# Kernel tuning notes

Measured on AMD Instinct MI355X. Metric: run time of the kernel, lower is better.

The kernel has to match this reference:

```python
import jax, jax.numpy as jnp
import numpy as np

N_NODES = 100000
N_EDGES = 3200000
HIDDEN = 128
N_CLASSES = 10
N_GRAPHS = 128
EPS = 1e-5


def setup_inputs() -> dict:
    key = jax.random.key(0)
    ks = jax.random.split(key, 16)
    x = jax.random.normal(ks[0], (N_NODES, 1), dtype=jnp.float32)
    edge_index = jax.random.randint(ks[1], (2, N_EDGES), 0, N_NODES, dtype=jnp.int64)
    batch = jnp.sort(jax.random.randint(ks[2], (N_NODES,), 0, N_GRAPHS, dtype=jnp.int64))
    def lin(k, fi, fo):
        s = 1.0 / np.sqrt(fi)
        return jax.random.uniform(k, (fi, fo), jnp.float32, -s, s)
    return {
        "x": x, "edge_index": edge_index, "batch": batch,
        "Wc1": lin(ks[3], 1, HIDDEN), "bc1": jnp.zeros((HIDDEN,), jnp.float32),
        "Wl1": lin(ks[4], 1, HIDDEN), "bl1": jnp.zeros((HIDDEN,), jnp.float32),
        "g1": jnp.ones((HIDDEN,), jnp.float32), "be1": jnp.zeros((HIDDEN,), jnp.float32),
        "Wc2": lin(ks[5], HIDDEN, HIDDEN), "bc2": jnp.zeros((HIDDEN,), jnp.float32),
        "Wl2": lin(ks[6], HIDDEN, HIDDEN), "bl2": jnp.zeros((HIDDEN,), jnp.float32),
        "g2": jnp.ones((HIDDEN,), jnp.float32), "be2": jnp.zeros((HIDDEN,), jnp.float32),
        "W3": lin(ks[7], HIDDEN, N_CLASSES), "b3": jnp.zeros((N_CLASSES,), jnp.float32),
    }


def _gcn_conv(x, W, b, src, dst, n):
    # PyG GCNConv: add self-loops, symmetric normalization, then scatter-add.
    h = x @ W                                    # [N, F]
    loops = jnp.arange(n, dtype=src.dtype)
    s = jnp.concatenate([src, loops])
    d = jnp.concatenate([dst, loops])
    deg = jax.ops.segment_sum(jnp.ones_like(d, dtype=h.dtype), d, num_segments=n)
    dinv = jnp.where(deg > 0, jax.lax.rsqrt(deg), 0.0)
    norm = dinv[s] * dinv[d]                     # [E+N]
    msg = h[s] * norm[:, None]                   # gather + scale
    out = jax.ops.segment_sum(msg, d, num_segments=n)
    return out + b


def _batch_norm(x, gamma, beta):
    mu = jnp.mean(x, axis=0)
    var = jnp.mean(jnp.square(x - mu), axis=0)
    return (x - mu) * jax.lax.rsqrt(var + EPS) * gamma + beta


def reference(x, edge_index, batch, Wc1, bc1, Wl1, bl1, g1, be1,
              Wc2, bc2, Wl2, bl2, g2, be2, W3, b3):
    src, dst = edge_index[0], edge_index[1]
    n = x.shape[0]
    h = _gcn_conv(x, Wc1, bc1, src, dst, n) + (x @ Wl1 + bl1)
    h = jax.nn.relu(h)
    h = _batch_norm(h, g1, be1)
    h = _gcn_conv(h, Wc2, bc2, src, dst, n) + (h @ Wl2 + bl2)
    h = _batch_norm(h, g2, be2)
    # global_mean_pool over graph ids
    sums = jax.ops.segment_sum(h, batch, num_segments=N_GRAPHS)
    cnts = jax.ops.segment_sum(jnp.ones((n,), h.dtype), batch, num_segments=N_GRAPHS)
    pooled = sums / jnp.maximum(cnts, 1.0)[:, None]
    return pooled @ W3 + b3
```

## Files before the change

kernel.cpp:

```cpp
#include <hip/hip_runtime.h>
#include <hip/hip_bf16.h>

__device__ __forceinline__ float bf2f(unsigned short u) {
    union { unsigned int i; float f; } c; c.i = ((unsigned int)u) << 16; return c.f;
}
__device__ __forceinline__ unsigned short f2bf(float f) {
    union { unsigned int i; float f; } c; c.f = f;
    unsigned int i = c.i;
    unsigned int r = (i + 0x7FFFu + ((i >> 16) & 1u)) >> 16;
    return (unsigned short)r;
}
__device__ __forceinline__ float u2f_hi(unsigned int u) {
    union { unsigned int i; float f; } c; c.i = u & 0xFFFF0000u; return c.f;
}
__device__ __forceinline__ float u2f_lo(unsigned int u) {
    union { unsigned int i; float f; } c; c.i = u << 16; return c.f;
}
__device__ __forceinline__ int ldi(const void* p, long long i, int is64) {
    return is64 ? (int)((const long long*)p)[i] : ((const int*)p)[i];
}

typedef __attribute__((ext_vector_type(8))) short short8;
typedef __attribute__((ext_vector_type(4))) float floatx4;

#define HID 128
#define EPS 1e-5f
#define NBK 256
#define CH 4096

#define OF_WC1 0
#define OF_BC1 128
#define OF_WL1 256
#define OF_BL1 384
#define OF_G1  512
#define OF_BE1 640
#define OF_WC2 768
#define OF_BC2 17152
#define OF_WL2 17280
#define OF_BL2 33664
#define OF_G2  33792
#define OF_BE2 33920
#define OF_W3  34048
#define OF_B3  35328
#define N_CANON 35338

__global__ void k_zero(int* __restrict__ p, long long n,
                       const unsigned int* __restrict__ g1w,
                       const unsigned int* __restrict__ eiw,
                       int* __restrict__ flags) {
    long long i = (long long)blockIdx.x * blockDim.x + threadIdx.x;
    if (i < n) p[i] = 0;
    if (blockIdx.x == 0 && threadIdx.x == 0) {
        flags[0] = (g1w[0] == 0x3F800000u) ? 1 : 0;
        flags[1] = (eiw[1] == 0u && eiw[3] == 0u && eiw[5] == 0u) ? 1 : 0;
    }
}

struct ConvArgs { const void* s[14]; float* d[14]; int n[14]; };
__global__ void k_wconv(ConvArgs a, const int* __restrict__ flags,
                        unsigned short* __restrict__ W2T) {
    int seg = blockIdx.y;
    int i = blockIdx.x * 256 + threadIdx.x;
    if (i >= a.n[seg]) return;
    float v = flags[0] ? ((const float*)a.s[seg])[i]
                       : bf2f(((const unsigned short*)a.s[seg])[i]);
    a.d[seg][i] = v;
    if (seg == 6) W2T[(i & 127) * 256 + (i >> 7)] = f2bf(v);
    else if (seg == 8) W2T[(i & 127) * 256 + 128 + (i >> 7)] = f2bf(v);
}


__global__ void __launch_bounds__(256) k_bhist(const void* __restrict__ ei, int E, int N,
                                               const int* __restrict__ flags,
                                               int* __restrict__ bcnt) {
    __shared__ int h[NBK];
    int t = threadIdx.x;
    h[t] = 0;
    __syncthreads();
    int is64 = flags[1];
    long long base = (long long)blockIdx.x * CH;
    for (int k = 0; k < CH / 256; k++) {
        long long i = base + k * 256 + t;
        if (i < E) {
            int d = ldi(ei, (long long)E + i, is64);
            if ((unsigned)d < (unsigned)N) atomicAdd(&h[d >> 9], 1);
        }
    }
    __syncthreads();
    if (h[t]) atomicAdd(&bcnt[t], h[t]);
}

__global__ void k_bscan(const int* __restrict__ bcnt, int* __restrict__ boff,
                        int* __restrict__ bcur) {
    __shared__ int sd[NBK];
    int t = threadIdx.x;
    int v = bcnt[t];
    sd[t] = v;
    __syncthreads();
    for (int off = 1; off < NBK; off <<= 1) {
        int add = (t >= off) ? sd[t - off] : 0;
        __syncthreads();
        sd[t] += add;
        __syncthreads();
    }
    int ex = sd[t] - v;
    boff[t] = ex;
    bcur[t] = ex;
}

__global__ void __launch_bounds__(256) k_bpart(const void* __restrict__ ei, int E, int N,
                                               const int* __restrict__ flags,
                                               int* __restrict__ bcur, uint2* __restrict__ pairs) {
    __shared__ uint2 buf[CH];
    __shared__ int h[NBK], sc[NBK], offs[NBK], cur[NBK], gpos[NBK];
    int t = threadIdx.x;
    h[t] = 0;
    __syncthreads();
    int is64 = flags[1];
    long long base = (long long)blockIdx.x * CH;
    int ss[CH / 256], dd[CH / 256];
    bool ok[CH / 256];
#pragma unroll
    for (int k = 0; k < CH / 256; k++) {
        long long i = base + k * 256 + t;
        ok[k] = false; ss[k] = 0; dd[k] = 0;
        if (i < E) {
            int s = ldi(ei, i, is64);
            int d = ldi(ei, (long long)E + i, is64);
            ss[k] = s; dd[k] = d;
            if ((unsigned)s < (unsigned)N && (unsigned)d < (unsigned)N) {
                ok[k] = true;
                atomicAdd(&h[d >> 9], 1);
            }
        }
    }
    __syncthreads();
    int hv = h[t];
    sc[t] = hv;
    __syncthreads();
    for (int off = 1; off < NBK; off <<= 1) {
        int add = (t >= off) ? sc[t - off] : 0;
        __syncthreads();
        sc[t] += add;
        __syncthreads();
    }
    offs[t] = sc[t] - hv;
    cur[t] = sc[t] - hv;
    __syncthreads();
#pragma unroll
    for (int k = 0; k < CH / 256; k++) {
        if (ok[k]) {
            int b = dd[k] >> 9;
            int p = atomicAdd(&cur[b], 1);
            buf[p] = make_uint2((unsigned)ss[k], (unsigned)dd[k]);
        }
    }
    if (hv) gpos[t] = atomicAdd(&bcur[t], hv);
    else gpos[t] = 0;
    __syncthreads();
    int vc = offs[NBK - 1] + h[NBK - 1];
    for (int i = t; i < vc; i += 256) {
        uint2 e = buf[i];
        int lo = (int)(e.y >> 9);
        pairs[(size_t)gpos[lo] + (i - offs[lo])] = e;
    }
}

__global__ void __launch_bounds__(256) k_bcsr(const uint2* __restrict__ pairs,
                                              const int* __restrict__ boff,
                                              const int* __restrict__ bcnt,
                                              const void* __restrict__ x,
                                              const int* __restrict__ flags,
                                              int N, int E,
                                              int* __restrict__ deg, int* __restrict__ rowptr,
                                              int* __restrict__ col,
                                              float* __restrict__ dinv, float* __restrict__ xf,
                                              float* __restrict__ xd1) {
    __shared__ int cnt[512], lofs[512], lcur[512], part[256];
    int b = blockIdx.x, t = threadIdx.x;
    for (int j = t; j < 512; j += 256) { cnt[j] = 0; lcur[j] = 0; }
    __syncthreads();
    int s0 = boff[b], n = bcnt[b];
    for (int i = t; i < n; i += 256) {
        uint2 p = pairs[(size_t)s0 + i];
        atomicAdd(&cnt[p.y & 511], 1);
    }
    __syncthreads();
    int a0 = cnt[2 * t], a1 = cnt[2 * t + 1];
    part[t] = a0 + a1;
    __syncthreads();
    for (int off = 1; off < 256; off <<= 1) {
        int add = (t >= off) ? part[t - off] : 0;
        __syncthreads();
        part[t] += add;
        __syncthreads();
    }
    int ex = part[t] - (a0 + a1);
    lofs[2 * t] = ex;
    lofs[2 * t + 1] = ex + a0;
    __syncthreads();
    int vb = b << 9;
    int isf32 = flags[0];
    for (int j = t; j < 512; j += 256) {
        int v = vb + j;
        if (v < N) {
            int dg = cnt[j];
            deg[v] = dg;
            rowptr[v] = s0 + lofs[j];
            float dv = rsqrtf((float)(dg + 1));
            float xv = isf32 ? ((const float*)x)[v] : bf2f(((const unsigned short*)x)[v]);
            dinv[v] = dv;
            xf[v] = xv;
            xd1[v] = xv * dv;
        }
    }
    for (int i = t; i < n; i += 256) {
        uint2 p = pairs[(size_t)s0 + i];
        int dl = p.y & 511;
        int sl = atomicAdd(&lcur[dl], 1);
        int idx = s0 + lofs[dl] + sl;
        if ((unsigned)idx < (unsigned)E) col[idx] = (int)p.x;
    }
}

__global__ void __launch_bounds__(256) k_bps(const uint2* __restrict__ pairs,
                                             const int* __restrict__ boff,
                                             const int* __restrict__ bcnt,
                                             const float* __restrict__ xd1,
                                             const float* __restrict__ xf,
                                             const float* __restrict__ dinv,
                                             const float* __restrict__ C,
                                             int N, float4* __restrict__ node,
                                             float* __restrict__ S1a, float* __restrict__ S2a) {
    __shared__ float psL[512], xL[512];
    int b = blockIdx.x, t = threadIdx.x;
    for (int j = t; j < 512; j += 256) psL[j] = 0.f;
    __syncthreads();
    int s0 = boff[b], n = bcnt[b];
    for (int i = t; i < n; i += 256) {
        uint2 p = pairs[(size_t)s0 + i];
        atomicAdd(&psL[p.y & 511], xd1[p.x]);
    }
    __syncthreads();
    int vb = b << 9;
    for (int j = t; j < 512; j += 256) {
        int v = vb + j;
        if (v < N) {
            float dv = dinv[v], xv = xf[v];
            float p = dv * (psL[j] + xv * dv);
            node[v] = make_float4(p, xv, dv, 0.f);
            psL[j] = p;
            xL[j] = xv;
        } else { psL[j] = 0.f; xL[j] = 0.f; }
    }
    __syncthreads();
    int f = t & 127, hh = t >> 7;
    float wc = C[OF_WC1 + f], wl = C[OF_WL1 + f];
    float bb = C[OF_BC1 + f] + C[OF_BL1 + f];
    int jend = min(512, N - vb);
    int j0 = hh * 256, j1 = min(j0 + 256, jend);
    float s1 = 0.f, s2 = 0.f;
    for (int j = j0; j < j1; j++) {
        float h = fmaxf(fmaf(psL[j], wc, fmaf(xL[j], wl, bb)), 0.f);
        s1 += h; s2 += h * h;
    }
    atomicAdd(&S1a[f], s1);
    atomicAdd(&S2a[f], s2);
}

#define RGF 32
__global__ void __launch_bounds__(256) k_fgg(
        const float4* __restrict__ node, const int* __restrict__ col,
        const int* __restrict__ rowptr, const int* __restrict__ deg,
        const float* __restrict__ S1a, const float* __restrict__ S2a,
        const unsigned short* __restrict__ W2T, const float* __restrict__ C,
        const void* __restrict__ batch, const int* __restrict__ flags,
        int N, int E,
        float* __restrict__ S1b, float* __restrict__ S2b, float* __restrict__ G) {
    __shared__ unsigned short azL[RGF * 264];
    int t = threadIdx.x;
    int wave = t >> 6, lane = t & 63;
    int vbase = blockIdx.x * RGF;
    int is64 = flags[1];
    if (vbase >= N) return;

    int f0 = 2 * lane, f1 = f0 + 1;
    float wc10 = C[OF_WC1 + f0], wl10 = C[OF_WL1 + f0];
    float wc11 = C[OF_WC1 + f1], wl11 = C[OF_WL1 + f1];
    float b10 = C[OF_BC1 + f0] + C[OF_BL1 + f0];
    float b11 = C[OF_BC1 + f1] + C[OF_BL1 + f1];
    float mu0 = S1a[f0] / (float)N;
    float var0 = S2a[f0] / (float)N - mu0 * mu0;
    float a10 = C[OF_G1 + f0] * rsqrtf(fmaxf(var0, 0.f) + EPS);
    float be10 = C[OF_BE1 + f0] - mu0 * a10;
    float mu1 = S1a[f1] / (float)N;
    float var1 = S2a[f1] / (float)N - mu1 * mu1;
    float a11 = C[OF_G1 + f1] * rsqrtf(fmaxf(var1, 0.f) + EPS);
    float be11 = C[OF_BE1 + f1] - mu1 * a11;

    auto zacc = [&](float4 n, float& a0, float& a1) {
        float z0 = fmaf(a10, fmaxf(fmaf(n.x, wc10, fmaf(n.y, wl10, b10)), 0.f), be10);
        float z1 = fmaf(a11, fmaxf(fmaf(n.x, wc11, fmaf(n.y, wl11, b11)), 0.f), be11);
        a0 = fmaf(n.z, z0, a0);
        a1 = fmaf(n.z, z1, a1);
    };

    for (int r = 0; r < 8; r++) {
        int row = wave * 8 + r;
        int v = vbase + row;
        unsigned aggp = 0, zp = 0;
        if (v < N) {
            float4 nv = node[v];
            float z0v = fmaf(a10, fmaxf(fmaf(nv.x, wc10, fmaf(nv.y, wl10, b10)), 0.f), be10);
            float z1v = fmaf(a11, fmaxf(fmaf(nv.x, wc11, fmaf(nv.y, wl11, b11)), 0.f), be11);
            float a0 = nv.z * z0v, a1 = nv.z * z1v;
            int base = max(rowptr[v], 0);
            int dn = max(0, min(deg[v], E - base));
            base = __builtin_amdgcn_readfirstlane(base);
            dn = __builtin_amdgcn_readfirstlane(dn);
            int j = 0;
            int head = min(dn, (4 - (base & 3)) & 3);
            for (; j < head; j++) {
                int s = col[base + j];
                if ((unsigned)s >= (unsigned)N) s = 0;
                zacc(node[s], a0, a1);
            }
            for (; j + 8 <= dn; j += 8) {
                int4 ca = *(const int4*)&col[base + j];
                int4 cb = *(const int4*)&col[base + j + 4];
                int s0 = ca.x, s1 = ca.y, s2 = ca.z, s3 = ca.w;
                int s4 = cb.x, s5 = cb.y, s6 = cb.z, s7 = cb.w;
                if ((unsigned)s0 >= (unsigned)N) s0 = 0;
                if ((unsigned)s1 >= (unsigned)N) s1 = 0;
                if ((unsigned)s2 >= (unsigned)N) s2 = 0;
                if ((unsigned)s3 >= (unsigned)N) s3 = 0;
                if ((unsigned)s4 >= (unsigned)N) s4 = 0;
                if ((unsigned)s5 >= (unsigned)N) s5 = 0;
                if ((unsigned)s6 >= (unsigned)N) s6 = 0;
                if ((unsigned)s7 >= (unsigned)N) s7 = 0;
                float4 n0 = node[s0], n1 = node[s1], n2 = node[s2], n3 = node[s3];
                float4 n4 = node[s4], n5 = node[s5], n6 = node[s6], n7 = node[s7];
                zacc(n0, a0, a1); zacc(n1, a0, a1); zacc(n2, a0, a1); zacc(n3, a0, a1);
                zacc(n4, a0, a1); zacc(n5, a0, a1); zacc(n6, a0, a1); zacc(n7, a0, a1);
            }
            for (; j + 4 <= dn; j += 4) {
                int4 cc = *(const int4*)&col[base + j];
                int s0 = cc.x, s1 = cc.y, s2 = cc.z, s3 = cc.w;
                if ((unsigned)s0 >= (unsigned)N) s0 = 0;
                if ((unsigned)s1 >= (unsigned)N) s1 = 0;
                if ((unsigned)s2 >= (unsigned)N) s2 = 0;
                if ((unsigned)s3 >= (unsigned)N) s3 = 0;
                float4 n0 = node[s0], n1 = node[s1], n2 = node[s2], n3 = node[s3];
                zacc(n0, a0, a1); zacc(n1, a0, a1); zacc(n2, a0, a1); zacc(n3, a0, a1);
            }
            for (; j < dn; j++) {
                int s = col[base + j];
                if ((unsigned)s >= (unsigned)N) s = 0;
                zacc(node[s], a0, a1);
            }
            aggp = (unsigned)f2bf(nv.z * a0) | ((unsigned)f2bf(nv.z * a1) << 16);
            zp   = (unsigned)f2bf(z0v) | ((unsigned)f2bf(z1v) << 16);
        }
        *(unsigned*)&azL[row * 264 + 2 * lane] = aggp;
        *(unsigned*)&azL[row * 264 + 128 + 2 * lane] = zp;
    }
    __syncthreads();

    int quad = lane >> 4, m = lane & 15;
    int half = wave >> 1, tg = wave & 1;
    int rbase = half * 16;
    short8 afr[8];
#pragma unroll
    for (int kb = 0; kb < 8; kb++)
        afr[kb] = *(const short8*)&azL[(rbase + m) * 264 + kb * 32 + quad * 8];

    int vlast = min(vbase + RGF - 1, N - 1);
    bool uni = (ldi(batch, vbase, is64) == ldi(batch, vlast, is64));

    float ps1[4], ps2[4], pgs[4];
#pragma unroll
    for (int ftl = 0; ftl < 4; ftl++) {
        int ft = tg * 4 + ftl;
        floatx4 acc = {0.f, 0.f, 0.f, 0.f};
        const unsigned short* brow = &W2T[(ft * 16 + m) * 256];
#pragma unroll
        for (int kb = 0; kb < 8; kb++) {
            short8 bfr = *(const short8*)&brow[kb * 32 + quad * 8];
            acc = __builtin_amdgcn_mfma_f32_16x16x32_bf16(afr[kb], bfr, acc, 0, 0, 0);
        }
        int cgl = ft * 16 + m;
        float bbv = C[OF_BC2 + cgl] + C[OF_BL2 + cgl];
        float s1 = 0.f, s2 = 0.f, gs = 0.f;
#pragma unroll
        for (int reg = 0; reg < 4; reg++) {
            int v = vbase + rbase + quad * 4 + reg;
            if (v < N) {
                float h = acc[reg] + bbv;
                s1 += h; s2 += h * h;
                if (uni) gs += h;
                else {
                    int g = ldi(batch, v, is64);
                    if ((unsigned)g < 128u) atomicAdd(&G[g * HID + cgl], h);
                }
            }
        }
        ps1[ftl] = s1; ps2[ftl] = s2; pgs[ftl] = gs;
    }

    __syncthreads();
    float* red = (float*)azL;
    int contrib = half * 4 + quad;
#pragma unroll
    for (int ftl = 0; ftl < 4; ftl++) {
        int cgl = (tg * 4 + ftl) * 16 + m;
        red[contrib * 128 + cgl]        = ps1[ftl];
        red[1024 + contrib * 128 + cgl] = ps2[ftl];
        red[2048 + contrib * 128 + cgl] = pgs[ftl];
    }
    __syncthreads();
    if (t < HID) {
        float a1 = 0.f, a2 = 0.f, ag = 0.f;
#pragma unroll
        for (int w = 0; w < 8; w++) {
            a1 += red[w * 128 + t];
            a2 += red[1024 + w * 128 + t];
            ag += red[2048 + w * 128 + t];
        }
        atomicAdd(&S1b[t], a1);
        atomicAdd(&S2b[t], a2);
        if (uni) {
            int g = ldi(batch, vbase, is64);
            if ((unsigned)g < 128u) atomicAdd(&G[g * HID + t], ag);
        }
    }
}

__global__ void k_prep(const void* __restrict__ x, const int* __restrict__ deg, int N,
                       const int* __restrict__ flags, float* __restrict__ dinv,
                       float* __restrict__ xf, float* __restrict__ xd1, float* __restrict__ rd) {
    int i = blockIdx.x * blockDim.x + threadIdx.x;
    if (i < N) {
        float dp1 = (float)(max(deg[i], 0) + 1);
        float dv = rsqrtf(dp1);
        float xv = flags[0] ? ((const float*)x)[i] : bf2f(((const unsigned short*)x)[i]);
        dinv[i] = dv;
        xf[i] = xv;
        xd1[i] = xv * dv;
        rd[i] = sqrtf(dp1);
    }
}

#define ROWS1 128
__global__ void k_stats1(const float4* __restrict__ node, const float* __restrict__ C,
                         int N, float* __restrict__ S1, float* __restrict__ S2) {
    int f = threadIdx.x;
    float wc = C[OF_WC1 + f], wl = C[OF_WL1 + f];
    float b = C[OF_BC1 + f] + C[OF_BL1 + f];
    int v0 = blockIdx.x * ROWS1;
    float s1 = 0.f, s2 = 0.f;
    for (int r = 0; r < ROWS1; r++) {
        int v = v0 + r;
        if (v >= N) break;
        float4 nd = node[v];
        float h = fmaxf(nd.x * wc + nd.y * wl + b, 0.f);
        s1 += h; s2 += h * h;
    }
    atomicAdd(&S1[f], s1);
    atomicAdd(&S2[f], s2);
}

__global__ void k_bn1(const float* __restrict__ S1, const float* __restrict__ S2,
                      const float* __restrict__ C, int N, float* __restrict__ ab) {
    int f = threadIdx.x;
    float mu = S1[f] / (float)N;
    float var = S2[f] / (float)N - mu * mu;
    float a = C[OF_G1 + f] * rsqrtf(fmaxf(var, 0.f) + EPS);
    ab[f] = a;
    ab[HID + f] = C[OF_BE1 + f] - mu * a;
}

__global__ void k_zmat(const float4* __restrict__ node, const float* __restrict__ C,
                       const float* __restrict__ ab, int N, unsigned int* __restrict__ zd) {
    int i = blockIdx.x * blockDim.x + threadIdx.x;
    if (i >= N * 64) return;
    int v = i >> 6, c = i & 63;
    float4 nd = node[v];
    int f0 = c * 2, f1 = f0 + 1;
    float z0 = ab[f0] * fmaxf(nd.x * C[OF_WC1 + f0] + nd.y * C[OF_WL1 + f0]
                              + C[OF_BC1 + f0] + C[OF_BL1 + f0], 0.f) + ab[HID + f0];
    float z1 = ab[f1] * fmaxf(nd.x * C[OF_WC1 + f1] + nd.y * C[OF_WL1 + f1]
                              + C[OF_BC1 + f1] + C[OF_BL1 + f1], 0.f) + ab[HID + f1];
    float dv = nd.z;
    zd[i] = (unsigned)f2bf(dv * z0) | ((unsigned)f2bf(dv * z1) << 16);
}

__global__ void __launch_bounds__(256) k_gather2(
        const unsigned int* __restrict__ zd, const int* __restrict__ col,
        const int* __restrict__ rowptr, const int* __restrict__ deg,
        const float* __restrict__ dinv, int N, int E, int c0r, int c1r,
        unsigned int* __restrict__ agg) {
    int gt = blockIdx.x * 256 + threadIdx.x;
    int w = gt >> 6, lane = gt & 63;
    int v = c0r + w;
    if (v >= c1r || v >= N) return;
    int base = max(rowptr[v], 0);
    int dn = max(0, min(deg[v], E - base));
    unsigned int us = zd[(size_t)v * 64 + lane];
    float a0 = u2f_lo(us), a1 = u2f_hi(us);
    for (int j = 0; j < dn; j++) {
        int s = col[base + j];
        if ((unsigned)s >= (unsigned)N) s = 0;
        unsigned int u = zd[(size_t)s * 64 + lane];
        a0 += u2f_lo(u); a1 += u2f_hi(u);
    }
    float dv = dinv[v];
    agg[(size_t)(v - c0r) * 64 + lane] = (unsigned)f2bf(dv * a0) | ((unsigned)f2bf(dv * a1) << 16);
}

#define RG 32
__global__ void __launch_bounds__(128) k_gemm3(
        const unsigned int* __restrict__ zd, const unsigned int* __restrict__ agg,
        const float* __restrict__ rd, const unsigned short* __restrict__ W2T,
        const float* __restrict__ C,
        const void* __restrict__ batch, const int* __restrict__ flags,
        int N, int c0r, int c1r,
        float* __restrict__ S1b, float* __restrict__ S2b, float* __restrict__ G) {
    __shared__ char smem[32 * 264 * 2];
    unsigned short* azL = (unsigned short*)smem;
    int t = threadIdx.x;
    int vbase = c0r + blockIdx.x * RG;
    int vend = min(c1r, N);
    int is64 = flags[1];
    if (vbase >= vend) return;

    for (int it = 0; it < 16; it++) {
        int idx = it * 128 + t;
        int r = idx >> 6, c = idx & 63;
        int v = vbase + r;
        unsigned ua = 0, uz = 0; float rv = 0.f;
        if (v < vend) {
            ua = agg[(size_t)(v - c0r) * 64 + c];
            uz = zd[(size_t)v * 64 + c];
            rv = rd[v];
        }
        *(unsigned*)&azL[r * 264 + 2 * c] = ua;
        float z0 = u2f_lo(uz) * rv, z1 = u2f_hi(uz) * rv;
        *(unsigned*)&azL[r * 264 + 128 + 2 * c] =
            (unsigned)f2bf(z0) | ((unsigned)f2bf(z1) << 16);
    }
    __syncthreads();

    int wave = t >> 6, lane = t & 63, quad = lane >> 4, m = lane & 15;

    short8 afr[8];
#pragma unroll
    for (int kb = 0; kb < 8; kb++)
        afr[kb] = *(const short8*)&azL[(wave * 16 + m) * 264 + kb * 32 + quad * 8];

    int vlast = min(vbase + RG - 1, vend - 1);
    bool uni = (ldi(batch, vbase, is64) == ldi(batch, vlast, is64));

    float ps1[8], ps2[8], pgs[8];
#pragma unroll
    for (int ft = 0; ft < 8; ft++) {
        floatx4 acc = {0.f, 0.f, 0.f, 0.f};
        const unsigned short* brow = &W2T[(ft * 16 + m) * 256];
#pragma unroll
        for (int kb = 0; kb < 8; kb++) {
            short8 bfr = *(const short8*)&brow[kb * 32 + quad * 8];
            acc = __builtin_amdgcn_mfma_f32_16x16x32_bf16(afr[kb], bfr, acc, 0, 0, 0);
        }
        int cgl = ft * 16 + m;
        float bbv = C[OF_BC2 + cgl] + C[OF_BL2 + cgl];
        float s1 = 0.f, s2 = 0.f, gs = 0.f;
#pragma unroll
        for (int reg = 0; reg < 4; reg++) {
            int v = vbase + wave * 16 + quad * 4 + reg;
            if (v < vend) {
                float h = acc[reg] + bbv;
                s1 += h; s2 += h * h;
                if (uni) gs += h;
                else {
                    int g = ldi(batch, v, is64);
                    if ((unsigned)g < 128u) atomicAdd(&G[g * HID + cgl], h);
                }
            }
        }
        ps1[ft] = s1; ps2[ft] = s2; pgs[ft] = gs;
    }

    __syncthreads();
    float* red = (float*)smem;
    int wq = wave * 4 + quad;
#pragma unroll
    for (int ft = 0; ft < 8; ft++) {
        int cgl = ft * 16 + m;
        red[wq * 128 + cgl]        = ps1[ft];
        red[1024 + wq * 128 + cgl] = ps2[ft];
        red[2048 + wq * 128 + cgl] = pgs[ft];
    }
    __syncthreads();
    if (t < HID) {
        float a1 = 0.f, a2 = 0.f, ag = 0.f;
#pragma unroll
        for (int w = 0; w < 8; w++) {
            a1 += red[w * 128 + t];
            a2 += red[1024 + w * 128 + t];
            ag += red[2048 + w * 128 + t];
        }
        atomicAdd(&S1b[t], a1);
        atomicAdd(&S2b[t], a2);
        if (uni) {
            int g = ldi(batch, vbase, is64);
            if ((unsigned)g < 128u) atomicAdd(&G[g * HID + t], ag);
        }
    }
}

__global__ void k_deg(const void* __restrict__ ei, int E, int N, const int* __restrict__ flags,
                      int* __restrict__ deg, int* __restrict__ slot) {
    int i = blockIdx.x * blockDim.x + threadIdx.x;
    if (i < E) {
        int d = ldi(ei, (long long)E + i, flags[1]);
        int sl = ((unsigned)d < (unsigned)N) ? atomicAdd(&deg[d], 1) : 0;
        slot[i] = sl;
    }
}
__global__ void k_scanA(const int* __restrict__ deg, int N, int* __restrict__ rowptr,
                        int* __restrict__ bsum) {
    __shared__ int sd[256];
    int t = threadIdx.x;
    int i = blockIdx.x * 256 + t;
    int my = (i < N) ? deg[i] : 0;
    sd[t] = my;
    __syncthreads();
    for (int off = 1; off < 256; off <<= 1) {
        int add = (t >= off) ? sd[t - off] : 0;
        __syncthreads();
        sd[t] += add;
        __syncthreads();
    }
    if (i < N) rowptr[i] = sd[t] - my;
    if (t == 255) bsum[blockIdx.x] = sd[255];
}
__global__ void k_scanB(int* __restrict__ bsum, int NB) {
    __shared__ int sd[512];
    int t = threadIdx.x;
    if (NB <= 512) {
        int v = (t < NB) ? bsum[t] : 0;
        sd[t] = v;
        __syncthreads();
        for (int off = 1; off < 512; off <<= 1) {
            int add = (t >= off) ? sd[t - off] : 0;
            __syncthreads();
            sd[t] += add;
            __syncthreads();
        }
        if (t < NB) bsum[t] = sd[t] - v;
    } else if (t == 0) {
        int run = 0;
        for (int b = 0; b < NB; b++) { int v = bsum[b]; bsum[b] = run; run += v; }
    }
}
__global__ void k_scanC(int* __restrict__ rowptr, const int* __restrict__ bsum, int N) {
    int i = blockIdx.x * blockDim.x + threadIdx.x;
    if (i < N) rowptr[i] += bsum[i >> 8];
}
__global__ void k_fill(const void* __restrict__ ei, int E, int N, const int* __restrict__ flags,
                       const int* __restrict__ rowptr, const int* __restrict__ slot,
                       int* __restrict__ col, const float* __restrict__ xd1,
                       float* __restrict__ ps) {
    int i = blockIdx.x * blockDim.x + threadIdx.x;
    if (i < E) {
        int is64 = flags[1];
        int s = ldi(ei, i, is64);
        int d = ldi(ei, (long long)E + i, is64);
        if ((unsigned)s < (unsigned)N && (unsigned)d < (unsigned)N) {
            int idx = rowptr[d] + slot[i];
            if ((unsigned)idx < (unsigned)E) col[idx] = s;
            atomicAdd(&ps[d], xd1[s]);
        }
    }
}
__global__ void k_node3(const float* __restrict__ xf, const float* __restrict__ ps,
                        const float* __restrict__ dinv, int N, float4* __restrict__ node) {
    int i = blockIdx.x * blockDim.x + threadIdx.x;
    if (i < N) {
        float dv = dinv[i];
        float xv = xf[i];
        node[i] = make_float4(dv * (ps[i] + xv * dv), xv, dv, 0.f);
    }
}

__global__ void k_out(const float* __restrict__ G,
                      const float* __restrict__ S1b, const float* __restrict__ S2b,
                      const float* __restrict__ C, const int* __restrict__ flags,
                      const void* __restrict__ batch,
                      int N, void* __restrict__ out) {
    __shared__ float pb[HID];
    int f = threadIdx.x;
    int g = blockIdx.x;
    int is64 = flags[1];
    auto lb = [&](int tv) {
        int lo = 0, hi = N;
        while (lo < hi) { int m = (lo + hi) >> 1; if (ldi(batch, m, is64) < tv) lo = m + 1; else hi = m; }
        return lo;
    };
    float cgc = fmaxf((float)(lb(g + 1) - lb(g)), 1.f);
    float mu = S1b[f] / (float)N;
    float var = S2b[f] / (float)N - mu * mu;
    float a = C[OF_G2 + f] * rsqrtf(fmaxf(var, 0.f) + EPS);
    float be = C[OF_BE2 + f] - mu * a;
    pb[f] = a * (G[g * HID + f] / cgc) + be;
    __syncthreads();
    if (f < 10) {
        float s = C[OF_B3 + f];
        for (int k = 0; k < HID; k++) s += pb[k] * C[OF_W3 + k * 10 + f];
        if (flags[0]) ((float*)out)[g * 10 + f] = s;
        else ((unsigned short*)out)[g * 10 + f] = f2bf(s);
    }
}

extern "C" void kernel_launch(void* const* d_in, const int* in_sizes, int n_in,
                              void* d_out, int out_size, void* d_ws, size_t ws_size,
                              hipStream_t stream) {
    const void* x   = d_in[0];
    const void* ei  = d_in[1];
    const void* bat = d_in[2];
    const void* w_src[14] = { d_in[3], d_in[4], d_in[5], d_in[6], d_in[7], d_in[8],
                              d_in[9], d_in[10], d_in[11], d_in[12], d_in[13], d_in[14],
                              d_in[15], d_in[16] };
    const int w_cnt[14] = { 128,128,128,128,128,128, 16384,128,16384,128,128,128, 1280,10 };

    const int N = in_sizes[0];
    const int E = in_sizes[1] / 2;
    const int NB = (N + 255) / 256;

    char* ws = (char*)d_ws;
    size_t off = 0;
    auto alloc = [&](size_t bytes) -> void* {
        void* p = ws + off;
        off = (off + bytes + 255) & ~(size_t)255;
        return p;
    };
    float* S1a  = (float*)alloc(HID * 4);
    float* S2a  = (float*)alloc(HID * 4);
    float* S1b  = (float*)alloc(HID * 4);
    float* S2b  = (float*)alloc(HID * 4);
    float* G    = (float*)alloc(128 * HID * 4);
    int*   bsum = (int*)  alloc(2048);
    int*   bcnt = (int*)  alloc(NBK * 4);
    size_t zbytes = off;
    int*    flags  = (int*)   alloc(256);
    float*  canon  = (float*) alloc(N_CANON * 4);
    unsigned short* W2T = (unsigned short*)alloc(HID * 256 * 2);
    float*  xf     = (float*) alloc((size_t)N * 4);
    float*  dinv   = (float*) alloc((size_t)N * 4);
    float*  xd1    = (float*) alloc((size_t)N * 4);
    float*  rd     = (float*) alloc((size_t)N * 4);
    float4* node   = (float4*)alloc((size_t)N * 16);
    int*    deg    = (int*)   alloc((size_t)N * 4);
    float*  ps     = (float*) alloc((size_t)N * 4);
    int*    rowptr = (int*)   alloc((size_t)N * 4);
    int*    boff   = (int*)   alloc(NBK * 4);
    int*    bcur   = (int*)   alloc(NBK * 4);
    float*  ab     = (float*) alloc(2 * HID * 4);
    size_t ebytes = ((size_t)E * 8 > (size_t)N * 256) ? (size_t)E * 8 : (size_t)N * 256;
    char*   edgebuf = (char*) alloc(ebytes);
    int*    col    = (int*)   alloc((size_t)E * 4);
    size_t fastNeed = off;
    unsigned int* zd = (unsigned int*)alloc((size_t)N * 256);
    unsigned int* aggSep = (unsigned int*)alloc((size_t)N * 256);
    size_t fbNeed = off;

    uint2* pairs = (uint2*)edgebuf;
    int* colFB = (int*)edgebuf;
    int* slotFB = (int*)(edgebuf + (size_t)E * 4);
    (void)n_in; (void)out_size;

    bool fastB = (ws_size >= fastNeed) && (N <= 131072);

    ConvArgs ca;
    int w_off[14] = { OF_WC1, OF_BC1, OF_WL1, OF_BL1, OF_G1, OF_BE1,
                      OF_WC2, OF_BC2, OF_WL2, OF_BL2, OF_G2, OF_BE2, OF_W3, OF_B3 };
    for (int i = 0; i < 14; i++) { ca.s[i] = w_src[i]; ca.d[i] = canon + w_off[i]; ca.n[i] = w_cnt[i]; }

    const int tb = 256;
    long long zn = (long long)(zbytes / 4);
    k_zero  <<<(int)((zn + tb - 1) / tb), tb, 0, stream>>>((int*)d_ws, zn,
                                                           (const unsigned int*)d_in[7],
                                                           (const unsigned int*)ei, flags);
    k_wconv <<<dim3(64, 14), 256, 0, stream>>>(ca, flags, W2T);

    if (fastB) {
        const int NCH = (E + CH - 1) / CH;
        const int nbk = (N + 511) >> 9;
        k_bhist<<<NCH, 256, 0, stream>>>(ei, E, N, flags, bcnt);
        k_bscan<<<1, NBK, 0, stream>>>(bcnt, boff, bcur);
        k_bpart<<<NCH, 256, 0, stream>>>(ei, E, N, flags, bcur, pairs);
        k_bcsr <<<nbk, 256, 0, stream>>>(pairs, boff, bcnt, x, flags, N, E,
                                         deg, rowptr, col, dinv, xf, xd1);
        k_bps  <<<nbk, 256, 0, stream>>>(pairs, boff, bcnt, xd1, xf, dinv, canon,
                                         N, node, S1a, S2a);
        k_fgg  <<<(N + RGF - 1) / RGF, 256, 0, stream>>>(node, col, rowptr, deg, S1a, S2a, W2T,
                                                         canon, bat, flags, N, E, S1b, S2b, G);
    } else {
        bool haveAgg = (ws_size >= fbNeed);
        unsigned int* agg = haveAgg ? aggSep : (unsigned int*)edgebuf;
        k_zero<<<(2 * N + tb - 1) / tb, tb, 0, stream>>>(deg, 2 * N,
                                                         (const unsigned int*)d_in[7],
                                                         (const unsigned int*)ei, flags);
        k_deg  <<<(E + tb - 1) / tb, tb, 0, stream>>>(ei, E, N, flags, deg, slotFB);
        k_prep <<<(N + tb - 1) / tb, tb, 0, stream>>>(x, deg, N, flags, dinv, xf, xd1, rd);
        k_scanA<<<NB, 256, 0, stream>>>(deg, N, rowptr, bsum);
        k_scanB<<<1, 512, 0, stream>>>(bsum, NB);
        k_scanC<<<NB, 256, 0, stream>>>(rowptr, bsum, N);
        k_fill <<<(E + tb - 1) / tb, tb, 0, stream>>>(ei, E, N, flags, rowptr, slotFB, colFB, xd1, ps);
        k_node3<<<(N + tb - 1) / tb, tb, 0, stream>>>(xf, ps, dinv, N, node);
        k_stats1<<<(N + ROWS1 - 1) / ROWS1, HID, 0, stream>>>(node, canon, N, S1a, S2a);
        k_bn1  <<<1, HID, 0, stream>>>(S1a, S2a, canon, N, ab);
        k_zmat <<<(N * 64 + tb - 1) / tb, tb, 0, stream>>>(node, canon, ab, N, zd);
        k_gather2<<<((size_t)N * 64 + tb - 1) / tb, tb, 0, stream>>>(zd, colFB, rowptr, deg, dinv,
                                                                     N, E, 0, N, agg);
        k_gemm3<<<(N + RG - 1) / RG, 128, 0, stream>>>(zd, agg, rd, W2T, canon, bat, flags,
                                                       N, 0, N, S1b, S2b, G);
    }
    k_out<<<128, HID, 0, stream>>>(G, S1b, S2b, canon, flags, bat, N, d_out);
}
```

Baseline: 429.5 us.

## Merge zero/convert/histogram kernels and use per-chunk offsets for edge partitioning

Fuses the workspace zeroing, weight conversion and bucket histogram into one launch, with each role chosen by block index. The histogram now stores per-chunk, per-bucket counts, so the scan kernel can compute deterministic per-chunk global offsets. The partition kernel then writes edges straight to global memory with only shared-memory atomics, dropping the LDS staging buffer and the second in-block scan. This removes two kernel launches and the global atomics, at the cost of a serial loop over chunks in the single-block scan and uncoalesced scattered global writes.

Result: slower. 587.7 us (+36.8%).

```diff
diff --git a/kernel.cpp b/kernel.cpp
--- a/kernel.cpp
+++ b/kernel.cpp
@@ -44,58 +44,68 @@
 #define OF_B3  35328
 #define N_CANON 35338
 
-__global__ void k_zero(int* __restrict__ p, long long n,
-                       const unsigned int* __restrict__ g1w,
-                       const unsigned int* __restrict__ eiw,
-                       int* __restrict__ flags) {
-    long long i = (long long)blockIdx.x * blockDim.x + threadIdx.x;
-    if (i < n) p[i] = 0;
-    if (blockIdx.x == 0 && threadIdx.x == 0) {
-        flags[0] = (g1w[0] == 0x3F800000u) ? 1 : 0;
-        flags[1] = (eiw[1] == 0u && eiw[3] == 0u && eiw[5] == 0u) ? 1 : 0;
-    }
-}
-
 struct ConvArgs { const void* s[14]; float* d[14]; int n[14]; };
-__global__ void k_wconv(ConvArgs a, const int* __restrict__ flags,
-                        unsigned short* __restrict__ W2T) {
-    int seg = blockIdx.y;
-    int i = blockIdx.x * 256 + threadIdx.x;
-    if (i >= a.n[seg]) return;
-    float v = flags[0] ? ((const float*)a.s[seg])[i]
-                       : bf2f(((const unsigned short*)a.s[seg])[i]);
-    a.d[seg][i] = v;
-    if (seg == 6) W2T[(i & 127) * 256 + (i >> 7)] = f2bf(v);
-    else if (seg == 8) W2T[(i & 127) * 256 + 128 + (i >> 7)] = f2bf(v);
-}
-
-
-__global__ void __launch_bounds__(256) k_bhist(const void* __restrict__ ei, int E, int N,
-                                               const int* __restrict__ flags,
-                                               int* __restrict__ bcnt) {
-    __shared__ int h[NBK];
-    int t = threadIdx.x;
-    h[t] = 0;
-    __syncthreads();
-    int is64 = flags[1];
-    long long base = (long long)blockIdx.x * CH;
-    for (int k = 0; k < CH / 256; k++) {
-        long long i = base + k * 256 + t;
-        if (i < E) {
-            int d = ldi(ei, (long long)E + i, is64);
-            if ((unsigned)d < (unsigned)N) atomicAdd(&h[d >> 9], 1);
-        }
-    }
-    __syncthreads();
-    if (h[t]) atomicAdd(&bcnt[t], h[t]);
-}
-
-__global__ void k_bscan(const int* __restrict__ bcnt, int* __restrict__ boff,
-                        int* __restrict__ bcur) {
+
+__global__ void __launch_bounds__(256) k_pre(int* __restrict__ p, long long n, int nz,
+                                             ConvArgs a, unsigned short* __restrict__ W2T,
+                                             const unsigned int* __restrict__ g1w,
+                                             const void* __restrict__ ei,
+                                             int E, int N, int nch,
+                                             int* __restrict__ chunkhist,
+                                             int* __restrict__ flags) {
+    int b = blockIdx.x, t = threadIdx.x;
+    if (b < nz) {
+        long long i = (long long)b * 256 + t;
+        if (i < n) p[i] = 0;
+        if (b == 0 && t == 0) {
+            const unsigned int* eiw = (const unsigned int*)ei;
+            flags[0] = (g1w[0] == 0x3F800000u) ? 1 : 0;
+            flags[1] = (eiw[1] == 0u && eiw[3] == 0u && eiw[5] == 0u) ? 1 : 0;
+        }
+        return;
+    }
+    b -= nz;
+    if (b < 896) {
+        int seg = b >> 6;
+        int i = (b & 63) * 256 + t;
+        if (i >= a.n[seg]) return;
+        bool isf32 = (g1w[0] == 0x3F800000u);
+        float v = isf32 ? ((const float*)a.s[seg])[i]
+                        : bf2f(((const unsigned short*)a.s[seg])[i]);
+        a.d[seg][i] = v;
+        if (seg == 6) W2T[(i & 127) * 256 + (i >> 7)] = f2bf(v);
+        else if (seg == 8) W2T[(i & 127) * 256 + 128 + (i >> 7)] = f2bf(v);
+        return;
+    }
+    b -= 896;
+    if (b < nch) {
+        __shared__ int h[NBK];
+        h[t] = 0;
+        __syncthreads();
+        const unsigned int* eiw = (const unsigned int*)ei;
+        int is64 = (eiw[1] == 0u && eiw[3] == 0u && eiw[5] == 0u) ? 1 : 0;
+        long long base = (long long)b * CH;
+        for (int k = 0; k < CH / 256; k++) {
+            long long i = base + k * 256 + t;
+            if (i < E) {
+                int s = ldi(ei, i, is64);
+                int d = ldi(ei, (long long)E + i, is64);
+                if ((unsigned)s < (unsigned)N && (unsigned)d < (unsigned)N)
+                    atomicAdd(&h[d >> 9], 1);
+            }
+        }
+        __syncthreads();
+        chunkhist[b * NBK + t] = h[t];
+    }
+}
+
+__global__ void k_bscan2(int* __restrict__ chunkhist, int nch,
+                         int* __restrict__ boff, int* __restrict__ bcnt) {
     __shared__ int sd[NBK];
     int t = threadIdx.x;
-    int v = bcnt[t];
-    sd[t] = v;
+    int tot = 0;
+    for (int c = 0; c < nch; c++) tot += chunkhist[c * NBK + t];
+    sd[t] = tot;
     __syncthreads();
     for (int off = 1; off < NBK; off <<= 1) {
         int add = (t >= off) ? sd[t - off] : 0;
@@ -103,66 +113,39 @@
         sd[t] += add;
         __syncthreads();
     }
-    int ex = sd[t] - v;
-    boff[t] = ex;
-    bcur[t] = ex;
-}
-
-__global__ void __launch_bounds__(256) k_bpart(const void* __restrict__ ei, int E, int N,
-                                               const int* __restrict__ flags,
-                                               int* __restrict__ bcur, uint2* __restrict__ pairs) {
-    __shared__ uint2 buf[CH];
-    __shared__ int h[NBK], sc[NBK], offs[NBK], cur[NBK], gpos[NBK];
-    int t = threadIdx.x;
-    h[t] = 0;
+    int run = sd[t] - tot;
+    boff[t] = run;
+    bcnt[t] = tot;
+    for (int c = 0; c < nch; c++) {
+        int v = chunkhist[c * NBK + t];
+        chunkhist[c * NBK + t] = run;
+        run += v;
+    }
+}
+
+__global__ void __launch_bounds__(256) k_bpart2(const void* __restrict__ ei, int E, int N,
+                                                const int* __restrict__ flags,
+                                                const int* __restrict__ gpos,
+                                                uint2* __restrict__ pairs) {
+    __shared__ int cur[NBK], gpL[NBK];
+    int t = threadIdx.x, c = blockIdx.x;
+    cur[t] = 0;
+    gpL[t] = gpos[c * NBK + t];
     __syncthreads();
     int is64 = flags[1];
-    long long base = (long long)blockIdx.x * CH;
-    int ss[CH / 256], dd[CH / 256];
-    bool ok[CH / 256];
-#pragma unroll
+    long long base = (long long)c * CH;
     for (int k = 0; k < CH / 256; k++) {
         long long i = base + k * 256 + t;
-        ok[k] = false; ss[k] = 0; dd[k] = 0;
         if (i < E) {
             int s = ldi(ei, i, is64);
             int d = ldi(ei, (long long)E + i, is64);
-            ss[k] = s; dd[k] = d;
             if ((unsigned)s < (unsigned)N && (unsigned)d < (unsigned)N) {
-                ok[k] = true;
-                atomicAdd(&h[d >> 9], 1);
+                int b = d >> 9;
+                int pos = gpL[b] + atomicAdd(&cur[b], 1);
+                if ((unsigned)pos < (unsigned)E)
+                    pairs[pos] = make_uint2((unsigned)s, (unsigned)d);
             }
         }
-    }
-    __syncthreads();
-    int hv = h[t];
-    sc[t] = hv;
-    __syncthreads();
-    for (int off = 1; off < NBK; off <<= 1) {
-        int add = (t >= off) ? sc[t - off] : 0;
-        __syncthreads();
-        sc[t] += add;
-        __syncthreads();
-    }
-    offs[t] = sc[t] - hv;
-    cur[t] = sc[t] - hv;
-    __syncthreads();
-#pragma unroll
-    for (int k = 0; k < CH / 256; k++) {
-        if (ok[k]) {
-            int b = dd[k] >> 9;
-            int p = atomicAdd(&cur[b], 1);
-            buf[p] = make_uint2((unsigned)ss[k], (unsigned)dd[k]);
-        }
-    }
-    if (hv) gpos[t] = atomicAdd(&bcur[t], hv);
-    else gpos[t] = 0;
-    __syncthreads();
-    int vc = offs[NBK - 1] + h[NBK - 1];
-    for (int i = t; i < vc; i += 256) {
-        uint2 e = buf[i];
-        int lo = (int)(e.y >> 9);
-        pairs[(size_t)gpos[lo] + (i - offs[lo])] = e;
     }
 }
 
@@ -450,6 +433,11 @@
     }
 }
 
+__global__ void k_zero2(int* __restrict__ p, long long n) {
+    long long i = (long long)blockIdx.x * blockDim.x + threadIdx.x;
+    if (i < n) p[i] = 0;
+}
+
 #define ROWS1 128
 __global__ void k_stats1(const float4* __restrict__ node, const float* __restrict__ C,
                          int N, float* __restrict__ S1, float* __restrict__ S2) {
@@ -735,6 +723,7 @@
     const int N = in_sizes[0];
     const int E = in_sizes[1] / 2;
     const int NB = (N + 255) / 256;
+    const int NCH = (E + CH - 1) / CH;
 
     char* ws = (char*)d_ws;
     size_t off = 0;
@@ -763,8 +752,8 @@
     float*  ps     = (float*) alloc((size_t)N * 4);
     int*    rowptr = (int*)   alloc((size_t)N * 4);
     int*    boff   = (int*)   alloc(NBK * 4);
-    int*    bcur   = (int*)   alloc(NBK * 4);
     float*  ab     = (float*) alloc(2 * HID * 4);
+    int*    chunkhist = (int*)alloc((size_t)NCH * NBK * 4);
     size_t ebytes = ((size_t)E * 8 > (size_t)N * 256) ? (size_t)E * 8 : (size_t)N * 256;
     char*   edgebuf = (char*) alloc(ebytes);
     int*    col    = (int*)   alloc((size_t)E * 4);
@@ -787,43 +776,42 @@
 
     const int tb = 256;
     long long zn = (long long)(zbytes / 4);
-    k_zero  <<<(int)((zn + tb - 1) / tb), tb, 0, stream>>>((int*)d_ws, zn,
-                                                           (const unsigned int*)d_in[7],
-                                                           (const unsigned int*)ei, flags);
-    k_wconv <<<dim3(64, 14), 256, 0, stream>>>(ca, flags, W2T);
+    const int nz = (int)((zn + tb - 1) / tb);
 
     if (fastB) {
-        const int NCH = (E + CH - 1) / CH;
         const int nbk = (N + 511) >> 9;
-        k_bhist<<<NCH, 256, 0, stream>>>(ei, E, N, flags, bcnt);
-        k_bscan<<<1, NBK, 0, stream>>>(bcnt, boff, bcur);
-        k_bpart<<<NCH, 256, 0, stream>>>(ei, E, N, flags, bcur, pairs);
-        k_bcsr <<<nbk, 256, 0, stream>>>(pairs, boff, bcnt, x, flags, N, E,
-                                         deg, rowptr, col, dinv, xf, xd1);
-        k_bps  <<<nbk, 256, 0, stream>>>(pairs, boff, bcnt, xd1, xf, dinv, canon,
-                                         N, node, S1a, S2a);
-        k_fgg  <<<(N + RGF - 1) / RGF, 256, 0, stream>>>(node, col, rowptr, deg, S1a, S2a, W2T,
-                                                         canon, bat, flags, N, E, S1b, S2b, G);
+        k_pre   <<<nz + 896 + NCH, 256, 0, stream>>>((int*)d_ws, zn, nz, ca, W2T,
+                                                     (const unsigned int*)d_in[7], ei,
+                                                     E, N, NCH, chunkhist, flags);
+        k_bscan2<<<1, NBK, 0, stream>>>(chunkhist, NCH, boff, bcnt);
+        k_bpart2<<<NCH, 256, 0, stream>>>(ei, E, N, flags, chunkhist, pairs);
+        k_bcsr  <<<nbk, 256, 0, stream>>>(pairs, boff, bcnt, x, flags, N, E,
+                                          deg, rowptr, col, dinv, xf, xd1);
+        k_bps   <<<nbk, 256, 0, stream>>>(pairs, boff, bcnt, xd1, xf, dinv, canon,
+                                          N, node, S1a, S2a);
+        k_fgg   <<<(N + RGF - 1) / RGF, 256, 0, stream>>>(node, col, rowptr, deg, S1a, S2a, W2T,
+                                                          canon, bat, flags, N, E, S1b, S2b, G);
     } else {
         bool haveAgg = (ws_size >= fbNeed);
         unsigned int* agg = haveAgg ? aggSep : (unsigned int*)edgebuf;
-        k_zero<<<(2 * N + tb - 1) / tb, tb, 0, stream>>>(deg, 2 * N,
-                                                         (const unsigned int*)d_in[7],
-                                                         (const unsigned int*)ei, flags);
-        k_deg  <<<(E + tb - 1) / tb, tb, 0, stream>>>(ei, E, N, flags, deg, slotFB);
-        k_prep <<<(N + tb - 1) / tb, tb, 0, stream>>>(x, deg, N, flags, dinv, xf, xd1, rd);
-        k_scanA<<<NB, 256, 0, stream>>>(deg, N, rowptr, bsum);
-        k_scanB<<<1, 512, 0, stream>>>(bsum, NB);
-        k_scanC<<<NB, 256, 0, stream>>>(rowptr, bsum, N);
-        k_fill <<<(E + tb - 1) / tb, tb, 0, stream>>>(ei, E, N, flags, rowptr, slotFB, colFB, xd1, ps);
-        k_node3<<<(N + tb - 1) / tb, tb, 0, stream>>>(xf, ps, dinv, N, node);
+        k_pre   <<<nz + 896, 256, 0, stream>>>((int*)d_ws, zn, nz, ca, W2T,
+                                               (const unsigned int*)d_in[7], ei,
+                                               E, N, 0, chunkhist, flags);
+        k_zero2 <<<(2 * N + tb - 1) / tb, tb, 0, stream>>>(deg, 2 * N);
+        k_deg   <<<(E + tb - 1) / tb, tb, 0, stream>>>(ei, E, N, flags, deg, slotFB);
+        k_prep  <<<(N + tb - 1) / tb, tb, 0, stream>>>(x, deg, N, flags, dinv, xf, xd1, rd);
+        k_scanA <<<NB, 256, 0, stream>>>(deg, N, rowptr, bsum);
+        k_scanB <<<1, 512, 0, stream>>>(bsum, NB);
+        k_scanC <<<NB, 256, 0, stream>>>(rowptr, bsum, N);
+        k_fill  <<<(E + tb - 1) / tb, tb, 0, stream>>>(ei, E, N, flags, rowptr, slotFB, colFB, xd1, ps);
+        k_node3 <<<(N + tb - 1) / tb, tb, 0, stream>>>(xf, ps, dinv, N, node);
         k_stats1<<<(N + ROWS1 - 1) / ROWS1, HID, 0, stream>>>(node, canon, N, S1a, S2a);
-        k_bn1  <<<1, HID, 0, stream>>>(S1a, S2a, canon, N, ab);
-        k_zmat <<<(N * 64 + tb - 1) / tb, tb, 0, stream>>>(node, canon, ab, N, zd);
+        k_bn1   <<<1, HID, 0, stream>>>(S1a, S2a, canon, N, ab);
+        k_zmat  <<<(N * 64 + tb - 1) / tb, tb, 0, stream>>>(node, canon, ab, N, zd);
         k_gather2<<<((size_t)N * 64 + tb - 1) / tb, tb, 0, stream>>>(zd, colFB, rowptr, deg, dinv,
                                                                      N, E, 0, N, agg);
-        k_gemm3<<<(N + RG - 1) / RG, 128, 0, stream>>>(zd, agg, rd, W2T, canon, bat, flags,
-                                                       N, 0, N, S1b, S2b, G);
+        k_gemm3 <<<(N + RG - 1) / RG, 128, 0, stream>>>(zd, agg, rd, W2T, canon, bat, flags,
+                                                        N, 0, N, S1b, S2b, G);
     }
     k_out<<<128, HID, 0, stream>>>(G, S1b, S2b, canon, flags, bat, N, d_out);
 }
```
